# Kernel optimization log

Hardware: AMD Instinct MI355X
Metric: run time of the kernel (lower is better)

## Reference

```python
import jax, jax.numpy as jnp
import numpy as np

N = 25600   # nodes
E = 409600  # edges (avg degree 16)
B = 64      # graphs in batch
NG = N // B # nodes per graph
D = 128     # node feature dim
H = 64      # hidden_size
L = 4       # num_labels
R = 32      # node rep dim (input_dim 64 = 2*R)


def setup_inputs():
    key = jax.random.key(0)
    ks = jax.random.split(key, 16)
    x = jax.random.normal(ks[0], (N, D), jnp.float32)
    # edges constrained to stay within each graph's node range
    src = jax.random.randint(ks[1], (E,), 0, N, dtype=jnp.int32)
    dst = (src // NG) * NG + jax.random.randint(ks[2], (E,), 0, NG, dtype=jnp.int32)
    edge_index = jnp.stack([src, dst])
    batch = (jnp.arange(N, dtype=jnp.int32) // NG)
    y = jax.random.randint(ks[3], (B,), 0, L, dtype=jnp.int32)
    state = (jnp.arange(E) % 2) == 0
    def w(k, shape):
        fan_in = shape[-2] if len(shape) > 1 else shape[0]
        return jax.random.normal(k, shape, jnp.float32) / np.sqrt(fan_in)
    params = dict(
        Wm1=w(ks[4], (D, H)), Wm2=w(ks[5], (H, R)), Wg=w(ks[6], (R, H)),
        W1=w(ks[7], (2 * R, 4 * H)), b1=jnp.zeros((4 * H,), jnp.float32),
        W2=w(ks[8], (4 * H, 2 * H)), b2=jnp.zeros((2 * H,), jnp.float32),
        W3=w(ks[9], (2 * H, H)), b3=jnp.zeros((H,), jnp.float32),
        We1=w(ks[10], (L, 2 * H, 2 * H)), be1=jnp.zeros((L, 2 * H), jnp.float32),
        We2=w(ks[11], (L, 2 * H, H)), be2=jnp.zeros((L, H), jnp.float32),
        We3=w(ks[12], (L, H, 1)), be3=jnp.zeros((L, 1), jnp.float32),
    )
    return dict(x=x, edge_index=edge_index, batch=batch, y=y, state=state, **params)


def _node_reps(x, src, dst, ew, Wm1, Wm2):
    # surrogate model.get_node_reps: one-hop message passing with edge weights ew
    h = jax.nn.elu(x @ Wm1)
    agg = jax.ops.segment_sum(h[src] * ew[:, None], dst, num_segments=N)
    return jax.nn.elu((h + agg) @ Wm2)


def _graph_rep(x, src, dst, ew, nmask, batch, Wm1, Wm2, Wg):
    # surrogate model.get_graph_rep: masked mean pooling of node reps
    nr = _node_reps(x, src, dst, ew, Wm1, Wm2)
    num = jax.ops.segment_sum(nr * nmask[:, None], batch, num_segments=B)
    cnt = jax.ops.segment_sum(nmask, batch, num_segments=B)
    pooled = num / jnp.maximum(cnt, 1.0)[:, None]  # zero for empty subgraphs
    return pooled @ Wg


def reference(x, edge_index, batch, y, state, Wm1, Wm2, Wg,
              W1, b1, W2, b2, W3, b3, We1, be1, We2, be2, We3, be3):
    src, dst = edge_index[0], edge_index[1]
    ones_e = jnp.ones((E,), x.dtype)
    graph_rep = _graph_rep(x, src, dst, ones_e, jnp.ones((N,), x.dtype), batch, Wm1, Wm2, Wg)
    # subgraph (occupied edges) rep: nodes incident to at least one occupied edge
    sf = state.astype(x.dtype)
    nmask = jnp.zeros((N,), x.dtype).at[src].max(sf).at[dst].max(sf)
    subgraph_rep = _graph_rep(x, src, dst, sf, nmask, batch, Wm1, Wm2, Wg)
    # available-edge node reps (message passing over available edges only)
    ava = ~state
    nr = _node_reps(x, src, dst, ava.astype(x.dtype), Wm1, Wm2)
    asrc = src[ava]
    adst = dst[ava]
    reps = jnp.concatenate([nr[asrc], nr[adst]], axis=1)  # [Ea, 2R]
    reps = jax.nn.elu(reps @ W1 + b1)
    reps = jax.nn.elu(reps @ W2 + b2)
    reps = reps @ W3 + b3  # [Ea, H]
    abatch = batch[asrc]
    ay = y[abatch]
    unique_batch = jnp.arange(B, dtype=batch.dtype)  # every graph has available edges by construction
    diff = (graph_rep - subgraph_rep)[abatch]  # [Ea, H]
    feats = jnp.concatenate([reps, diff], axis=1)  # [Ea, 2H]
    # per-label explainer MLPs, batched over labels
    h1 = jax.nn.elu(jnp.einsum('ef,lfg->leg', feats, We1) + be1[:, None, :])
    h2 = jax.nn.elu(jnp.einsum('leg,lgh->leh', h1, We2) + be2[:, None, :])
    scores = (jnp.einsum('leh,lho->leo', h2, We3) + be3[:, None, :])[..., 0].T  # [Ea, L]
    probs = jnp.take_along_axis(scores, ay[:, None], axis=1)[:, 0]  # [Ea]
    # scatter_max over graphs: values + argmax edge index
    seg_max = jax.ops.segment_max(probs, abatch, num_segments=B)
    idx = jnp.arange(probs.shape[0])
    added_actions = jax.ops.segment_min(
        jnp.where(probs == seg_max[abatch], idx, probs.shape[0]), abatch, num_segments=B)
    return probs, seg_max, added_actions, unique_batch
```

## Files before the change

kernel.cpp:

```cpp
#include <hip/hip_runtime.h>

#define NN 25600
#define EE 409600
#define BB 64
#define NGR 400
#define DD 128
#define HH 64
#define RR 32
#define EA 204800

#define OFF_AGGE   0
#define OFF_AGGO   1638400
#define OFF_NMASK  3276800
#define OFF_POOLF  3302400
#define OFF_POOLS  3304448
#define OFF_CNT    3306496
#define OFF_LCOUNT 3306560
#define OFF_CNT2   3306696
#define ZERO_END   3306824
#define OFF_H      3306824
#define OFF_NRA    4945224
#define OFF_BIAS1  5764424
#define OFF_ELIST  5772616
#define OFF_SEGKEYP 300000

typedef short bf16x8 __attribute__((ext_vector_type(8)));
typedef float floatx4 __attribute__((ext_vector_type(4)));
#define MFMA16 __builtin_amdgcn_mfma_f32_16x16x32_bf16

__device__ __forceinline__ float eluf(float v){ return v > 0.f ? v : __expf(v) - 1.f; }

__device__ __forceinline__ void splitbf(float v, unsigned short& h, unsigned short& l){
  const unsigned u = __float_as_uint(v);
  h = (unsigned short)(u >> 16);
  const float hf = __uint_as_float(u & 0xFFFF0000u);
  l = (unsigned short)(__float_as_uint(v - hf) >> 16);
}
__device__ __forceinline__ float bf2f(unsigned short s){
  return __uint_as_float(((unsigned)s) << 16);
}

__device__ __forceinline__ unsigned long long packkey(float f, unsigned idx){
  unsigned u = __float_as_uint(f);
  u = (u & 0x80000000u) ? ~u : (u | 0x80000000u);
  return ((unsigned long long)u << 32) | (unsigned long long)(0xFFFFFFFFu - idx);
}

__global__ __launch_bounds__(256) void k_hb(const float* __restrict__ x,
                                            const float* __restrict__ Wm1,
                                            float* __restrict__ h,
                                            const int* __restrict__ ei,
                                            const int* __restrict__ y,
                                            unsigned* __restrict__ lcount,
                                            int* __restrict__ elist,
                                            unsigned* __restrict__ cnt2,
                                            int* __restrict__ elist2)
{
  const int tid = threadIdx.x;
  if (blockIdx.x < 400){
    __shared__ float xs[64][129];
    const int n0 = blockIdx.x * 64;
    for (int idx = tid; idx < 64*128; idx += 256){
      int r = idx >> 7, c = idx & 127;
      xs[r][c] = x[(n0 + r)*DD + c];
    }
    __syncthreads();
    const int m = tid & 63, ng = tid >> 6;
    float4 acc[4];
    #pragma unroll
    for (int c = 0; c < 4; ++c) acc[c] = make_float4(0.f,0.f,0.f,0.f);
    for (int k = 0; k < 128; ++k){
      const float a = xs[m][k];
      const float* wr = Wm1 + k*64 + ng*16;
      #pragma unroll
      for (int c = 0; c < 4; ++c){
        const float4 w = *(const float4*)(wr + 4*c);
        acc[c].x += a*w.x; acc[c].y += a*w.y; acc[c].z += a*w.z; acc[c].w += a*w.w;
      }
    }
    float* hp = h + (n0 + m)*HH + ng*16;
    #pragma unroll
    for (int c = 0; c < 4; ++c){
      hp[4*c+0] = eluf(acc[c].x); hp[4*c+1] = eluf(acc[c].y);
      hp[4*c+2] = eluf(acc[c].z); hp[4*c+3] = eluf(acc[c].w);
    }
  } else {
    __shared__ unsigned cl[128], bl[128], ol[128];
    __shared__ unsigned lc[4], lb[4], lo[4];
    const int e0 = (blockIdx.x - 400) * (EE/256);
    if (tid < 128){ cl[tid] = 0; ol[tid] = 0; }
    if (tid < 4){ lc[tid] = 0; lo[tid] = 0; }
    __syncthreads();
    int bk[7]; int ne = 0;
    for (int e = e0 + tid; e < e0 + EE/256; e += 256){
      const int d = ei[EE + e];
      const int g = d / NGR;
      const int bkt = g*2 + (e & 1);
      bk[ne++] = bkt;
      atomicAdd(&cl[bkt], 1u);
      if (e & 1) atomicAdd(&lc[y[g]], 1u);
    }
    __syncthreads();
    if (tid < 128 && cl[tid]) bl[tid] = atomicAdd(&cnt2[tid], cl[tid]);
    if (tid < 4 && lc[tid])   lb[tid] = atomicAdd(&lcount[tid], lc[tid]);
    __syncthreads();
    ne = 0;
    for (int e = e0 + tid; e < e0 + EE/256; e += 256){
      const int bkt = bk[ne++];
      const int s = ei[e];
      const int d = ei[EE + e];
      const unsigned r = atomicAdd(&ol[bkt], 1u);
      elist2[bkt*4096 + (int)(bl[bkt] + r)] = (s << 9) | (d - (bkt >> 1)*NGR);
      if (e & 1){
        const int l = y[bkt >> 1];
        const unsigned r2 = atomicAdd(&lo[l], 1u);
        elist[l*EA + (int)(lb[l] + r2)] = e >> 1;
      }
    }
  }
}

__global__ __launch_bounds__(256) void k_edges(const float* __restrict__ h,
                                               const unsigned* __restrict__ cnt2,
                                               const int* __restrict__ elist2,
                                               float* __restrict__ aggE,
                                               float* __restrict__ aggO,
                                               float* __restrict__ nmask)
{
  __shared__ float acc[400*20];
  __shared__ unsigned char mk[400];
  const int b = blockIdx.x;
  const int g = b >> 3, p = (b >> 2) & 1, ch = b & 3;
  const int tid = threadIdx.x;
  const int nlo = g * NGR;
  for (int i = tid; i < 400*20; i += 256) acc[i] = 0.f;
  if (tid < 400) mk[tid] = 0;
  __syncthreads();
  const int bkt = g*2 + p;
  const int n = (int)cnt2[bkt];
  const int j0 = tid >> 2, c4 = tid & 3;
  const bool domask = (p == 0) && (ch == 0) && (c4 == 0);
  const int* el = elist2 + bkt*4096;
  int j = j0;
  for (; j + 64 < n; j += 128){
    const int w0 = el[j];
    const int w1 = el[j + 64];
    const int s0 = w0 >> 9, d0 = w0 & 511;
    const int s1 = w1 >> 9, d1 = w1 & 511;
    const float4 v0 = *(const float4*)(h + s0*HH + ch*16 + c4*4);
    const float4 v1 = *(const float4*)(h + s1*HH + ch*16 + c4*4);
    float* a0 = &acc[d0*20 + c4*4];
    atomicAdd(a0+0, v0.x); atomicAdd(a0+1, v0.y);
    atomicAdd(a0+2, v0.z); atomicAdd(a0+3, v0.w);
    float* a1 = &acc[d1*20 + c4*4];
    atomicAdd(a1+0, v1.x); atomicAdd(a1+1, v1.y);
    atomicAdd(a1+2, v1.z); atomicAdd(a1+3, v1.w);
    if (domask){ mk[s0 - nlo] = 1; mk[d0] = 1; mk[s1 - nlo] = 1; mk[d1] = 1; }
  }
  if (j < n){
    const int w0 = el[j];
    const int s0 = w0 >> 9, d0 = w0 & 511;
    const float4 v0 = *(const float4*)(h + s0*HH + ch*16 + c4*4);
    float* a0 = &acc[d0*20 + c4*4];
    atomicAdd(a0+0, v0.x); atomicAdd(a0+1, v0.y);
    atomicAdd(a0+2, v0.z); atomicAdd(a0+3, v0.w);
    if (domask){ mk[s0 - nlo] = 1; mk[d0] = 1; }
  }
  __syncthreads();
  float* agg = p ? aggO : aggE;
  for (int idx = tid; idx < 400*16; idx += 256){
    const int d = idx >> 4, col = idx & 15;
    agg[(nlo + d)*HH + ch*16 + col] = acc[d*20 + col];
  }
  if (p == 0 && ch == 0){
    for (int idx = tid; idx < 400; idx += 256) nmask[nlo + idx] = (float)mk[idx];
  }
}

__global__ __launch_bounds__(256) void k_node(const float* __restrict__ h,
                                              const float* __restrict__ aggE,
                                              const float* __restrict__ aggO,
                                              const float* __restrict__ Wm2,
                                              const float* __restrict__ nmask,
                                              float* __restrict__ nra,
                                              float* __restrict__ poolF,
                                              float* __restrict__ poolS,
                                              float* __restrict__ cntArr)
{
  __shared__ float hs[8][64], ae[8][64], ao[8][64];
  __shared__ float wm[64][32];
  __shared__ float rf[8][32], rs[8][32], rc[8];
  const int tid = threadIdx.x;
  const int n0 = blockIdx.x * 8;
  for (int idx = tid; idx < 512; idx += 256){
    int i = idx >> 6, k = idx & 63, n = n0 + i;
    hs[i][k] = h[n*HH + k];
    ae[i][k] = aggE[n*HH + k];
    ao[i][k] = aggO[n*HH + k];
  }
  for (int idx = tid; idx < 2048; idx += 256) wm[idx >> 5][idx & 31] = Wm2[idx];
  __syncthreads();
  const int i = tid >> 5, r = tid & 31;
  const int n = n0 + i;
  float aF = 0.f, aS = 0.f, aA = 0.f;
  #pragma unroll 4
  for (int k = 0; k < 64; ++k){
    const float th = hs[i][k], te = ae[i][k], to = ao[i][k], w = wm[k][r];
    aF += (th + te + to) * w;
    aS += (th + te) * w;
    aA += (th + to) * w;
  }
  aF = eluf(aF); aS = eluf(aS); aA = eluf(aA);
  nra[n*RR + r] = aA;
  const float msk = nmask[n];
  rf[i][r] = aF;
  rs[i][r] = (msk != 0.f) ? aS : 0.f;
  if (r == 0) rc[i] = (msk != 0.f) ? 1.f : 0.f;
  __syncthreads();
  const int g = n0 / NGR;
  if (tid < 32){
    float sf = 0.f, ss = 0.f;
    #pragma unroll
    for (int k = 0; k < 8; ++k){ sf += rf[k][tid]; ss += rs[k][tid]; }
    atomicAdd(&poolF[g*RR + tid], sf);
    atomicAdd(&poolS[g*RR + tid], ss);
  } else if (tid == 32){
    float sc = 0.f;
    #pragma unroll
    for (int k = 0; k < 8; ++k) sc += rc[k];
    atomicAdd(&cntArr[g], sc);
  }
}

__global__ __launch_bounds__(256) void k_pg(const float* __restrict__ W1,
                                            const float* __restrict__ W2,
                                            const float* __restrict__ W3,
                                            const float* __restrict__ We1,
                                            const float* __restrict__ We2,
                                            unsigned short* __restrict__ pk,
                                            const float* __restrict__ poolF,
                                            const float* __restrict__ poolS,
                                            const float* __restrict__ cnt,
                                            const float* __restrict__ Wg,
                                            const int* __restrict__ y,
                                            const float* __restrict__ be1,
                                            const float* __restrict__ b3,
                                            float* __restrict__ bias1,
                                            unsigned long long* __restrict__ segp)
{
  const int tid = threadIdx.x;
  if (blockIdx.x < 72){
    const int t = blockIdx.x*4 + (tid >> 6);
    const int L = tid & 63;
    unsigned short* dh = pk + (unsigned)t*1024 + L*8;
    unsigned short* dl = dh + 512;
    if (t >= 96 && t < 224){
      const int u = t - 96;
      const int lb = u >> 5, tl = u & 31;
      const int nt = tl >> 2, kt = tl & 3;
      const int krow = kt*32 + (L >> 4)*8;
      const int col  = nt*16 + (L & 15);
      float v[8];
      #pragma unroll
      for (int j = 0; j < 8; ++j) v[j] = 0.f;
      const float* werow = We1 + lb*16384 + col;
      #pragma unroll 4
      for (int m = 0; m < 64; ++m){
        const float we = werow[m*128];
        #pragma unroll
        for (int j = 0; j < 8; ++j) v[j] += W3[(krow + j)*64 + m] * we;
      }
      #pragma unroll
      for (int j = 0; j < 8; ++j){
        unsigned short h, l2;
        splitbf(v[j], h, l2);
        dh[j] = h; dl[j] = l2;
      }
      return;
    }
    int tl, KT, N; const float* W;
    if (t < 32)      { tl = t;      KT = 2; N = 256; W = W1; }
    else if (t < 96) { tl = t-32;   KT = 8; N = 128; W = W2; }
    else             { int u = t-224; int lb = u >> 4; tl = u & 15; KT = 4; N = 64;  W = We2 + lb*8192; }
    const int nt = tl / KT, kt = tl % KT;
    const int krow = kt*32 + (L >> 4)*8;
    const int col  = nt*16 + (L & 15);
    #pragma unroll
    for (int j = 0; j < 8; ++j){
      const float v = W[(krow + j)*N + col];
      unsigned short h, l2;
      splitbf(v, h, l2);
      dh[j] = h; dl[j] = l2;
    }
  } else {
    __shared__ float pd[32];
    __shared__ float dg[64];
    const int g = blockIdx.x - 72;
    if (g == 0 && tid < 128){
      #pragma unroll
      for (int k = 0; k < 4; ++k) segp[tid*4 + k] = 0ull;
    }
    if (tid < 32){
      const float c = cnt[g];
      const float pf = poolF[g*RR + tid] * (1.0f/400.0f);
      const float ps = poolS[g*RR + tid] / fmaxf(c, 1.0f);
      pd[tid] = pf - ps;
    }
    __syncthreads();
    if (tid < 64){
      float a = 0.f;
      #pragma unroll
      for (int r = 0; r < 32; ++r) a += pd[r] * Wg[r*64 + tid];
      dg[tid] = a;
    }
    __syncthreads();
    if (tid < 128){
      const int l = y[g];
      float acc = be1[l*128 + tid];
      #pragma unroll 8
      for (int j = 0; j < 64; ++j) acc += dg[j] * We1[l*16384 + (64 + j)*128 + tid];
      #pragma unroll 8
      for (int j = 0; j < 64; ++j) acc += b3[j] * We1[l*16384 + j*128 + tid];
      bias1[g*128 + tid] = acc;
    }
  }
}

template<int NTW,int KT,int MS,bool DOELU,int SIN,int SOUT,bool ROWBIAS>
__device__ __forceinline__ void layerR(const unsigned short (*__restrict__ Ih)[SIN],
                                       const unsigned short (*__restrict__ Il)[SIN],
                                       unsigned short (*__restrict__ Oh)[SOUT],
                                       unsigned short (*__restrict__ Ol)[SOUT],
                                       const bf16x8 (&BH)[NTW][KT],
                                       const bf16x8 (&BL)[NTW][KT],
                                       const float* __restrict__ bias,
                                       const int* __restrict__ gA,
                                       int colBase, int rowBase, int lane)
{
  const int c = lane & 15, q = lane >> 4;
  floatx4 acc[MS][NTW];
  #pragma unroll
  for (int ms = 0; ms < MS; ++ms){
    #pragma unroll
    for (int nt = 0; nt < NTW; ++nt){
      const int col = colBase + nt*16 + c;
      if (ROWBIAS){
        #pragma unroll
        for (int r = 0; r < 4; ++r)
          acc[ms][nt][r] = bias[gA[rowBase + ms*16 + q*4 + r]*128 + col];
      } else {
        const float bv = bias[col];
        acc[ms][nt][0]=bv; acc[ms][nt][1]=bv; acc[ms][nt][2]=bv; acc[ms][nt][3]=bv;
      }
    }
  }
  #pragma unroll
  for (int kt = 0; kt < KT; ++kt){
    bf16x8 ah[MS], al[MS];
    #pragma unroll
    for (int ms = 0; ms < MS; ++ms){
      ah[ms] = *(const bf16x8*)&Ih[rowBase + ms*16 + c][kt*32 + q*8];
      al[ms] = *(const bf16x8*)&Il[rowBase + ms*16 + c][kt*32 + q*8];
    }
    #pragma unroll
    for (int nt = 0; nt < NTW; ++nt){
      #pragma unroll
      for (int ms = 0; ms < MS; ++ms){
        acc[ms][nt] = MFMA16(ah[ms], BH[nt][kt], acc[ms][nt], 0, 0, 0);
        acc[ms][nt] = MFMA16(al[ms], BH[nt][kt], acc[ms][nt], 0, 0, 0);
        acc[ms][nt] = MFMA16(ah[ms], BL[nt][kt], acc[ms][nt], 0, 0, 0);
      }
    }
  }
  #pragma unroll
  for (int ms = 0; ms < MS; ++ms){
    #pragma unroll
    for (int nt = 0; nt < NTW; ++nt){
      const int col = colBase + nt*16 + c;
      #pragma unroll
      for (int r = 0; r < 4; ++r){
        float v = acc[ms][nt][r];
        if (DOELU) v = eluf(v);
        unsigned short h, l2;
        splitbf(v, h, l2);
        const int row = rowBase + ms*16 + q*4 + r;
        Oh[row][col] = h; Ol[row][col] = l2;
      }
    }
  }
}

__global__ __launch_bounds__(512, 1) void k_mlp(const float* __restrict__ nra,
                                             const int* __restrict__ ei,
                                             const unsigned short* __restrict__ pk,
                                             const float* __restrict__ b1,
                                             const float* __restrict__ b2,
                                             const float* __restrict__ be2,
                                             const float* __restrict__ We3,
                                             const float* __restrict__ be3,
                                             const float* __restrict__ bias1,
                                             const int* __restrict__ elist,
                                             const unsigned* __restrict__ lcount,
                                             float* __restrict__ probs,
                                             unsigned long long* __restrict__ segp)
{
  __shared__ unsigned short Xh[64][264], Xl[64][264];
  __shared__ unsigned short Yh[64][136], Yl[64][136];
  __shared__ int iA[64], gA[64];
  __shared__ unsigned long long lmax[64];
  const int tid = threadIdx.x;
  const int wv = tid >> 6, lane = tid & 63;

  if (tid < 64) lmax[tid] = 0ull;

  const unsigned c0 = lcount[0], c1 = lcount[1], c2 = lcount[2], c3 = lcount[3];
  const int t0 = (int)((c0+63)>>6), t1 = (int)((c1+63)>>6), t2 = (int)((c2+63)>>6), t3 = (int)((c3+63)>>6);
  const int ttot = t0 + t1 + t2 + t3;

  bf16x8 w1h[2][2], w1l[2][2];
  #pragma unroll
  for (int nt = 0; nt < 2; ++nt){
    #pragma unroll
    for (int kt = 0; kt < 2; ++kt){
      const unsigned short* bp = pk + (unsigned)(((wv*2 + nt)*2 + kt)*1024) + lane*8;
      w1h[nt][kt] = *(const bf16x8*)bp;
      w1l[nt][kt] = *(const bf16x8*)(bp + 512);
    }
  }
  bf16x8 w2h[1][8], w2l[1][8];
  #pragma unroll
  for (int kt = 0; kt < 8; ++kt){
    const unsigned short* bp = pk + (unsigned)((32 + wv*8 + kt)*1024) + lane*8;
    w2h[0][kt] = *(const bf16x8*)bp;
    w2l[0][kt] = *(const bf16x8*)(bp + 512);
  }
  bf16x8 w3h[1][4], w3l[1][4], w4h[1][4], w4l[1][4];
  int lcur = -1;

  for (int j = blockIdx.x; j < ttot; j += 256){
    int l, t; unsigned cnt;
    if      (j < t0)       { l = 0; t = j;          cnt = c0; }
    else if (j < t0+t1)    { l = 1; t = j-t0;       cnt = c1; }
    else if (j < t0+t1+t2) { l = 2; t = j-t0-t1;    cnt = c2; }
    else                   { l = 3; t = j-t0-t1-t2; cnt = c3; }
    if (l != lcur){
      lcur = l;
      #pragma unroll
      for (int kt = 0; kt < 4; ++kt){
        const unsigned short* bp = pk + (unsigned)((96 + l*32 + wv*4 + kt)*1024) + lane*8;
        w3h[0][kt] = *(const bf16x8*)bp;
        w3l[0][kt] = *(const bf16x8*)(bp + 512);
        const unsigned short* bq = pk + (unsigned)((224 + l*16 + (wv&3)*4 + kt)*1024) + lane*8;
        w4h[0][kt] = *(const bf16x8*)bq;
        w4l[0][kt] = *(const bf16x8*)(bq + 512);
      }
    }
    const int base = t * 64;
    const int valid = min(64, (int)(cnt - (unsigned)base));

    if (tid < 64){
      const int mm = (tid < valid) ? tid : 0;
      const int i = elist[l*EA + base + mm];
      const int e = 2*i + 1;
      iA[tid] = i; gA[tid] = ei[e] / NGR;
    }
    {
      const int m = tid >> 3, t8 = tid & 7;
      const int mm = (m < valid) ? m : 0;
      const int i = elist[l*EA + base + mm];
      const int e = 2*i + 1;
      const int node = (t8 < 4) ? ei[e] : ei[EE + e];
      const int off = (t8 & 3) * 8;
      const float* np_ = nra + node*RR + off;
      const int cb = ((t8 < 4) ? 0 : 32) + off;
      #pragma unroll
      for (int jj = 0; jj < 8; ++jj){
        unsigned short h, l2;
        splitbf(np_[jj], h, l2);
        Yh[m][cb + jj] = h; Yl[m][cb + jj] = l2;
      }
    }
    __syncthreads();
    layerR<2,2,4,true ,136,264,false>(Yh,Yl,Xh,Xl, w1h,w1l, b1,         gA, wv*32,      0,          lane);
    __syncthreads();
    layerR<1,8,4,true ,264,136,false>(Xh,Xl,Yh,Yl, w2h,w2l, b2,         gA, wv*16,      0,          lane);
    __syncthreads();
    layerR<1,4,4,true ,136,264,true >(Yh,Yl,Xh,Xl, w3h,w3l, bias1,      gA, wv*16,      0,          lane);
    __syncthreads();
    layerR<1,4,2,true ,264,136,false>(Xh,Xl,Yh,Yl, w4h,w4l, be2 + l*64, gA, (wv&3)*16, (wv>>2)*32, lane);
    __syncthreads();
    if (tid < 256){
      const int m = tid >> 2, part = tid & 3;
      const float* w3p = We3 + l*64 + part*16;
      const unsigned short* xh = &Yh[m][part*16];
      const unsigned short* xl = &Yl[m][part*16];
      float s = 0.f;
      #pragma unroll
      for (int kk = 0; kk < 16; ++kk)
        s += (bf2f(xh[kk]) + bf2f(xl[kk])) * w3p[kk];
      s += __shfl_down(s, 2);
      s += __shfl_down(s, 1);
      if (part == 0 && m < valid){
        s += be3[l];
        const int i = iA[m];
        probs[i] = s;
        atomicMax(&lmax[gA[m]], packkey(s, (unsigned)i));
      }
    }
    __syncthreads();
  }
  __syncthreads();
  if (tid < 64){
    const unsigned long long k = lmax[tid];
    if (k) atomicMax(&segp[tid*8], k);
  }
}

__global__ void k_final(const unsigned long long* __restrict__ segp, float* __restrict__ out)
{
  const int g = threadIdx.x;
  if (g < BB){
    const unsigned long long key = segp[g*8];
    const unsigned u = (unsigned)(key >> 32);
    const float mx = (u & 0x80000000u) ? __uint_as_float(u & 0x7FFFFFFFu)
                                       : __uint_as_float(~u);
    const unsigned idx = 0xFFFFFFFFu - (unsigned)(key & 0xFFFFFFFFull);
    out[EA + g]        = mx;
    out[EA + BB + g]   = (float)idx;
    out[EA + 2*BB + g] = (float)g;
  }
}

extern "C" void kernel_launch(void* const* d_in, const int* in_sizes, int n_in,
                              void* d_out, int out_size, void* d_ws, size_t ws_size,
                              hipStream_t stream)
{
  (void)in_sizes; (void)n_in; (void)out_size; (void)ws_size;
  const float* x   = (const float*)d_in[0];
  const int*   ei  = (const int*)  d_in[1];
  const int*   y   = (const int*)  d_in[3];
  const float* Wm1 = (const float*)d_in[5];
  const float* Wm2 = (const float*)d_in[6];
  const float* Wg  = (const float*)d_in[7];
  const float* W1  = (const float*)d_in[8];
  const float* b1  = (const float*)d_in[9];
  const float* W2  = (const float*)d_in[10];
  const float* b2  = (const float*)d_in[11];
  const float* W3  = (const float*)d_in[12];
  const float* b3  = (const float*)d_in[13];
  const float* We1 = (const float*)d_in[14];
  const float* be1 = (const float*)d_in[15];
  const float* We2 = (const float*)d_in[16];
  const float* be2 = (const float*)d_in[17];
  const float* We3 = (const float*)d_in[18];
  const float* be3 = (const float*)d_in[19];

  float* wsf = (float*)d_ws;
  float* AGGE   = wsf + OFF_AGGE;
  float* AGGO   = wsf + OFF_AGGO;
  float* NMASK  = wsf + OFF_NMASK;
  float* POOLF  = wsf + OFF_POOLF;
  float* POOLS  = wsf + OFF_POOLS;
  float* CNT    = wsf + OFF_CNT;
  unsigned* LCOUNT = (unsigned*)(wsf + OFF_LCOUNT);
  unsigned* CNT2 = (unsigned*)(wsf + OFF_CNT2);
  float* Hbuf   = wsf + OFF_H;
  float* NRA    = wsf + OFF_NRA;
  float* BIAS1  = wsf + OFF_BIAS1;
  int*   ELIST  = (int*)(wsf + OFF_ELIST);
  int*   ELIST2 = (int*)(wsf + OFF_NRA);
  unsigned short* PK = (unsigned short*)(wsf + OFF_AGGE);
  unsigned long long* SEGP = (unsigned long long*)(wsf + OFF_SEGKEYP);
  float* out = (float*)d_out;

  hipMemsetAsync(wsf + OFF_POOLF, 0, (size_t)(ZERO_END - OFF_POOLF) * sizeof(float), stream);

  k_hb    <<<656,     256, 0, stream>>>(x, Wm1, Hbuf, ei, y, LCOUNT, ELIST, CNT2, ELIST2);
  k_edges <<<BB*8,    256, 0, stream>>>(Hbuf, CNT2, ELIST2, AGGE, AGGO, NMASK);
  k_node  <<<NN/8,    256, 0, stream>>>(Hbuf, AGGE, AGGO, Wm2, NMASK, NRA, POOLF, POOLS, CNT);
  k_pg    <<<136,     256, 0, stream>>>(W1, W2, W3, We1, We2, PK,
                                        POOLF, POOLS, CNT, Wg, y, be1, b3, BIAS1, SEGP);
  k_mlp   <<<256,     512, 0, stream>>>(NRA, ei, PK, b1, b2, be2, We3, be3,
                                        BIAS1, ELIST, LCOUNT, out, SEGP);
  k_final <<<1,        64, 0, stream>>>(SEGP, out);
}
```

Baseline: 458.4 us.

## Retile per-wave MLP work into a 4x2 wave grid with more N-tiles

```diff
diff --git a/kernel.cpp b/kernel.cpp
--- a/kernel.cpp
+++ b/kernel.cpp
@@ -410,6 +410,7 @@
   __shared__ unsigned long long lmax[64];
   const int tid = threadIdx.x;
   const int wv = tid >> 6, lane = tid & 63;
+  const int wvn = wv & 3, wvm = wv >> 2;
 
   if (tid < 64) lmax[tid] = 0ull;
 
@@ -417,24 +418,27 @@
   const int t0 = (int)((c0+63)>>6), t1 = (int)((c1+63)>>6), t2 = (int)((c2+63)>>6), t3 = (int)((c3+63)>>6);
   const int ttot = t0 + t1 + t2 + t3;
 
-  bf16x8 w1h[2][2], w1l[2][2];
+  bf16x8 w1h[4][2], w1l[4][2];
+  #pragma unroll
+  for (int nt = 0; nt < 4; ++nt){
+    #pragma unroll
+    for (int kt = 0; kt < 2; ++kt){
+      const unsigned short* bp = pk + (unsigned)(((wvn*4 + nt)*2 + kt)*1024) + lane*8;
+      w1h[nt][kt] = *(const bf16x8*)bp;
+      w1l[nt][kt] = *(const bf16x8*)(bp + 512);
+    }
+  }
+  bf16x8 w2h[2][8], w2l[2][8];
   #pragma unroll
   for (int nt = 0; nt < 2; ++nt){
     #pragma unroll
-    for (int kt = 0; kt < 2; ++kt){
-      const unsigned short* bp = pk + (unsigned)(((wv*2 + nt)*2 + kt)*1024) + lane*8;
-      w1h[nt][kt] = *(const bf16x8*)bp;
-      w1l[nt][kt] = *(const bf16x8*)(bp + 512);
-    }
-  }
-  bf16x8 w2h[1][8], w2l[1][8];
-  #pragma unroll
-  for (int kt = 0; kt < 8; ++kt){
-    const unsigned short* bp = pk + (unsigned)((32 + wv*8 + kt)*1024) + lane*8;
-    w2h[0][kt] = *(const bf16x8*)bp;
-    w2l[0][kt] = *(const bf16x8*)(bp + 512);
-  }
-  bf16x8 w3h[1][4], w3l[1][4], w4h[1][4], w4l[1][4];
+    for (int kt = 0; kt < 8; ++kt){
+      const unsigned short* bp = pk + (unsigned)((32 + (wvn*2 + nt)*8 + kt)*1024) + lane*8;
+      w2h[nt][kt] = *(const bf16x8*)bp;
+      w2l[nt][kt] = *(const bf16x8*)(bp + 512);
+    }
+  }
+  bf16x8 w3h[2][4], w3l[2][4], w4h[1][4], w4l[1][4];
   int lcur = -1;
 
   for (int j = blockIdx.x; j < ttot; j += 256){
@@ -446,11 +450,17 @@
     if (l != lcur){
       lcur = l;
       #pragma unroll
+      for (int nt = 0; nt < 2; ++nt){
+        #pragma unroll
+        for (int kt = 0; kt < 4; ++kt){
+          const unsigned short* bp = pk + (unsigned)((96 + l*32 + (wvn*2 + nt)*4 + kt)*1024) + lane*8;
+          w3h[nt][kt] = *(const bf16x8*)bp;
+          w3l[nt][kt] = *(const bf16x8*)(bp + 512);
+        }
+      }
+      #pragma unroll
       for (int kt = 0; kt < 4; ++kt){
-        const unsigned short* bp = pk + (unsigned)((96 + l*32 + wv*4 + kt)*1024) + lane*8;
-        w3h[0][kt] = *(const bf16x8*)bp;
-        w3l[0][kt] = *(const bf16x8*)(bp + 512);
-        const unsigned short* bq = pk + (unsigned)((224 + l*16 + (wv&3)*4 + kt)*1024) + lane*8;
+        const unsigned short* bq = pk + (unsigned)((224 + l*16 + wvn*4 + kt)*1024) + lane*8;
         w4h[0][kt] = *(const bf16x8*)bq;
         w4l[0][kt] = *(const bf16x8*)(bq + 512);
       }
@@ -481,13 +491,13 @@
       }
     }
     __syncthreads();
-    layerR<2,2,4,true ,136,264,false>(Yh,Yl,Xh,Xl, w1h,w1l, b1,         gA, wv*32,      0,          lane);
-    __syncthreads();
-    layerR<1,8,4,true ,264,136,false>(Xh,Xl,Yh,Yl, w2h,w2l, b2,         gA, wv*16,      0,          lane);
-    __syncthreads();
-    layerR<1,4,4,true ,136,264,true >(Yh,Yl,Xh,Xl, w3h,w3l, bias1,      gA, wv*16,      0,          lane);
-    __syncthreads();
-    layerR<1,4,2,true ,264,136,false>(Xh,Xl,Yh,Yl, w4h,w4l, be2 + l*64, gA, (wv&3)*16, (wv>>2)*32, lane);
+    layerR<4,2,2,true ,136,264,false>(Yh,Yl,Xh,Xl, w1h,w1l, b1,         gA, wvn*64, wvm*32, lane);
+    __syncthreads();
+    layerR<2,8,2,true ,264,136,false>(Xh,Xl,Yh,Yl, w2h,w2l, b2,         gA, wvn*32, wvm*32, lane);
+    __syncthreads();
+    layerR<2,4,2,true ,136,264,true >(Yh,Yl,Xh,Xl, w3h,w3l, bias1,      gA, wvn*32, wvm*32, lane);
+    __syncthreads();
+    layerR<1,4,2,true ,264,136,false>(Xh,Xl,Yh,Yl, w4h,w4l, be2 + l*64, gA, wvn*16, wvm*32, lane);
     __syncthreads();
     if (tid < 256){
       const int m = tid >> 2, part = tid & 3;
```

New measurement: 577.3 us. +26.0%, slower.
